# Kernel optimization log

Hardware: AMD Instinct MI355X
Metric: run time of the kernel (lower is better)

The kernel has to match this reference:

```python
import jax, jax.numpy as jnp
import numpy as np

NEG_SLOPE = 0.2
N_NODES = 50000


def gatv2_layer(x, src, dst, Wl, Wr, att, b, concat):
    # GATv2Conv (PyG semantics): x_l = lin_l(x) feeds messages (source side),
    # x_r = lin_r(x) is the target side; attention logit per edge/head is
    # att . leaky_relu(x_l[src] + x_r[dst]); softmax over incoming edges of dst.
    H, C = att.shape
    n = x.shape[0]
    xl = (x @ Wl).reshape(n, H, C)   # [N,H,C]
    xr = (x @ Wr).reshape(n, H, C)
    h = xl[src] + xr[dst]            # [E,H,C] gather
    logits = jnp.einsum('ehc,hc->eh', jax.nn.leaky_relu(h, NEG_SLOPE), att)  # [E,H]
    # segment softmax over target nodes
    m = jax.ops.segment_max(logits, dst, num_segments=n)
    m = jnp.where(jnp.isfinite(m), m, 0.0)
    ex = jnp.exp(logits - m[dst])
    s = jax.ops.segment_sum(ex, dst, num_segments=n)
    alpha = ex / (s[dst] + 1e-16)    # [E,H]
    msg = xl[src] * alpha[:, :, None]               # [E,H,C]
    out = jax.ops.segment_sum(msg, dst, num_segments=n)  # [N,H,C] scatter-add
    out = out.reshape(n, H * C) if concat else out.mean(axis=1)
    return out + b


def setup_inputs() -> dict:
    key = jax.random.key(0)
    ks = jax.random.split(key, 10)
    in_c, out_c, heads = 128, 64, 2
    node_fts = jax.random.normal(ks[0], (N_NODES, in_c), dtype=jnp.float32)
    edge_index = jax.random.randint(ks[1], (2, 800000), 0, N_NODES, dtype=jnp.int64)
    sc = 0.1
    return {
        'node_fts': node_fts,
        'edge_index': edge_index,
        'Wl1': jax.random.normal(ks[2], (in_c, heads * out_c), dtype=jnp.float32) * sc,
        'Wr1': jax.random.normal(ks[3], (in_c, heads * out_c), dtype=jnp.float32) * sc,
        'att1': jax.random.normal(ks[4], (heads, out_c), dtype=jnp.float32) * sc,
        'b1': jnp.zeros((heads * out_c,), dtype=jnp.float32),
        'Wl2': jax.random.normal(ks[5], (heads * out_c, out_c), dtype=jnp.float32) * sc,
        'Wr2': jax.random.normal(ks[6], (heads * out_c, out_c), dtype=jnp.float32) * sc,
        'att2': jax.random.normal(ks[7], (1, out_c), dtype=jnp.float32) * sc,
        'b2': jnp.zeros((out_c,), dtype=jnp.float32),
    }


def reference(node_fts, edge_index, Wl1, Wr1, att1, b1, Wl2, Wr2, att2, b2):
    n = node_fts.shape[0]
    loop = jnp.arange(n, dtype=edge_index.dtype)  # add_self_loops=True default
    src = jnp.concatenate([edge_index[0], loop])
    dst = jnp.concatenate([edge_index[1], loop])
    x = gatv2_layer(node_fts, src, dst, Wl1, Wr1, att1, b1, concat=True)
    x = jax.nn.relu(x)
    x = gatv2_layer(x, src, dst, Wl2, Wr2, att2, b2, concat=False)
    x = jax.nn.relu(x)
    return x
```

## Files before the change

### kernel.cpp

```cpp
#include <hip/hip_runtime.h>
#include <math.h>

typedef unsigned short ush;
typedef short bf16x8 __attribute__((ext_vector_type(8)));
typedef float f32x4 __attribute__((ext_vector_type(4)));
typedef ush ushx8 __attribute__((ext_vector_type(8)));

__device__ __forceinline__ ush f2bf(float f) {
    unsigned u = __float_as_uint(f);
    u += 0x7FFFu + ((u >> 16) & 1u);
    return (ush)(u >> 16);
}
__device__ __forceinline__ float bf2f(ush u) {
    return __uint_as_float((unsigned)u << 16);
}

__global__ __launch_bounds__(64) void prep_w_k(
    const float* __restrict__ Wl1, const float* __restrict__ Wr1,
    const float* __restrict__ Wl2, const float* __restrict__ Wr2,
    ush* __restrict__ wph, ush* __restrict__ wpl) {
    const int bid = blockIdx.x, l = threadIdx.x;
    const float* W;
    int C, fid;
    if (bid < 32)      { W = Wl1; C = 128; fid = bid; }
    else if (bid < 64) { W = Wr1; C = 128; fid = bid - 32; }
    else if (bid < 80) { W = Wl2; C = 64;  fid = bid - 64; }
    else               { W = Wr2; C = 64;  fid = bid - 80; }
    const int nc16 = C / 16;
    const int ks = fid / nc16, c16 = fid % nc16;
#pragma unroll
    for (int j = 0; j < 8; ++j) {
        const int k = ks * 32 + (l >> 4) * 8 + j;
        const int c = c16 * 16 + (l & 15);
        const float v = W[(size_t)k * C + c];
        const ush h = f2bf(v);
        wph[(size_t)(bid * 64 + l) * 8 + j] = h;
        wpl[(size_t)(bid * 64 + l) * 8 + j] = f2bf(v - bf2f(h));
    }
}

__global__ __launch_bounds__(256) void gemm1_k(
    const float* __restrict__ x,
    const ush* __restrict__ wh1, const ush* __restrict__ wl1,
    const ush* __restrict__ wh2, const ush* __restrict__ wl2,
    ush* __restrict__ ybf, float* __restrict__ yf, int n) {
    const int l = threadIdx.x & 63;
    const int w = threadIdx.x >> 6;
    const int r0 = blockIdx.x * 64 + w * 16;
    const int arow = min(r0 + (l & 15), n - 1);
    const int kb = (l >> 4) * 8;

    bf16x8 ah[4], al[4];
#pragma unroll
    for (int ks = 0; ks < 4; ++ks) {
        const float* ap = x + (size_t)arow * 128 + ks * 32 + kb;
        const float4 v0 = *reinterpret_cast<const float4*>(ap);
        const float4 v1 = *reinterpret_cast<const float4*>(ap + 4);
        const float fv[8] = {v0.x, v0.y, v0.z, v0.w, v1.x, v1.y, v1.z, v1.w};
#pragma unroll
        for (int j = 0; j < 8; ++j) {
            const ush h = f2bf(fv[j]);
            ah[ks][j] = (short)h;
            al[ks][j] = (short)f2bf(fv[j] - bf2f(h));
        }
    }
    const int drow = (l >> 4) * 4;
    const int dcol = l & 15;
#pragma unroll
    for (int slab = 0; slab < 4; ++slab) {
        const bool isW1 = slab < 2;
        const int sl = slab & 1;
        const ush* __restrict__ wh = isW1 ? wh1 : wh2;
        const ush* __restrict__ wl = isW1 ? wl1 : wl2;
#pragma unroll
        for (int c16 = 0; c16 < 4; ++c16) {
            f32x4 acc = {0.f, 0.f, 0.f, 0.f};
#pragma unroll
            for (int ks = 0; ks < 4; ++ks) {
                const int fid = ks * 8 + sl * 4 + c16;
                const bf16x8 bh = *reinterpret_cast<const bf16x8*>(wh + (size_t)(fid * 64 + l) * 8);
                const bf16x8 bl = *reinterpret_cast<const bf16x8*>(wl + (size_t)(fid * 64 + l) * 8);
                acc = __builtin_amdgcn_mfma_f32_16x16x32_bf16(ah[ks], bh, acc, 0, 0, 0);
                acc = __builtin_amdgcn_mfma_f32_16x16x32_bf16(al[ks], bh, acc, 0, 0, 0);
                acc = __builtin_amdgcn_mfma_f32_16x16x32_bf16(ah[ks], bl, acc, 0, 0, 0);
            }
            const int cg = sl * 64 + c16 * 16 + dcol;
#pragma unroll
            for (int q = 0; q < 4; ++q) {
                const int gr = r0 + drow + q;
                if (gr < n) {
                    if (isW1) ybf[(size_t)gr * 128 + cg] = f2bf(acc[q]);
                    else      yf[(size_t)gr * 128 + cg] = acc[q];
                }
            }
        }
    }
}

__global__ __launch_bounds__(256) void gemm2_k(
    const ush* __restrict__ ahi, const ush* __restrict__ alo,
    const ush* __restrict__ whl, const ush* __restrict__ wll,
    const ush* __restrict__ whr, const ush* __restrict__ wlr,
    ush* __restrict__ ybf, float* __restrict__ yf, int n) {
    const int l = threadIdx.x & 63;
    const int w = threadIdx.x >> 6;
    const int r0 = blockIdx.x * 64 + w * 16;
    const int arow = min(r0 + (l & 15), n - 1);
    const int kb = (l >> 4) * 8;
    bf16x8 ah[4], al[4];
#pragma unroll
    for (int ks = 0; ks < 4; ++ks) {
        ah[ks] = *reinterpret_cast<const bf16x8*>(ahi + (size_t)arow * 128 + ks * 32 + kb);
        al[ks] = *reinterpret_cast<const bf16x8*>(alo + (size_t)arow * 128 + ks * 32 + kb);
    }
    const int drow = (l >> 4) * 4;
    const int dcol = l & 15;
#pragma unroll
    for (int slab = 0; slab < 2; ++slab) {
        const ush* __restrict__ wh = slab ? whr : whl;
        const ush* __restrict__ wl = slab ? wlr : wll;
#pragma unroll
        for (int c16 = 0; c16 < 4; ++c16) {
            f32x4 acc = {0.f, 0.f, 0.f, 0.f};
#pragma unroll
            for (int ks = 0; ks < 4; ++ks) {
                const int fid = ks * 4 + c16;
                const bf16x8 bh = *reinterpret_cast<const bf16x8*>(wh + (size_t)(fid * 64 + l) * 8);
                const bf16x8 bl = *reinterpret_cast<const bf16x8*>(wl + (size_t)(fid * 64 + l) * 8);
                acc = __builtin_amdgcn_mfma_f32_16x16x32_bf16(ah[ks], bh, acc, 0, 0, 0);
                acc = __builtin_amdgcn_mfma_f32_16x16x32_bf16(al[ks], bh, acc, 0, 0, 0);
                acc = __builtin_amdgcn_mfma_f32_16x16x32_bf16(ah[ks], bl, acc, 0, 0, 0);
            }
            const int cg = c16 * 16 + dcol;
#pragma unroll
            for (int q = 0; q < 4; ++q) {
                const int gr = r0 + drow + q;
                if (gr < n) {
                    if (slab == 0) ybf[(size_t)gr * 64 + cg] = f2bf(acc[q]);
                    else           yf[(size_t)gr * 64 + cg] = acc[q];
                }
            }
        }
    }
}

__global__ __launch_bounds__(256) void hist_k(const int* __restrict__ dsts,
                                              int* __restrict__ ghist,
                                              int e0, int etot) {
    __shared__ int h[512];
    const int t = threadIdx.x;
    for (int i = t; i < 512; i += 256) h[i] = 0;
    __syncthreads();
    for (int i = blockIdx.x * blockDim.x + t; i < etot; i += gridDim.x * blockDim.x) {
        const int d = (i < e0) ? dsts[i] : (i - e0);
        atomicAdd(&h[d >> 7], 1);
    }
    __syncthreads();
    for (int i = t; i < 512; i += 256)
        if (h[i]) atomicAdd(&ghist[i], h[i]);
}

__global__ __launch_bounds__(512) void scanb_k(const int* __restrict__ ghist,
                                               int* __restrict__ boff,
                                               int* __restrict__ cur) {
    __shared__ int red[512];
    const int t = threadIdx.x;
    const int x = ghist[t];
    red[t] = x;
    __syncthreads();
#pragma unroll
    for (int s = 1; s < 512; s <<= 1) {
        const int add = (t >= s) ? red[t - s] : 0;
        __syncthreads();
        red[t] += add;
        __syncthreads();
    }
    const int excl = red[t] - x;
    boff[t] = excl;
    cur[t] = excl;
}

__global__ __launch_bounds__(256) void semisort_k(
    const int* __restrict__ srcs, const int* __restrict__ dsts,
    int* __restrict__ cur, int* __restrict__ pairs, int e0, int etot) {
    __shared__ int hist[512], gbase[512], lcur[512];
    const int t = threadIdx.x;
    const int start = blockIdx.x * 2048;
    const int end = min(start + 2048, etot);
    for (int i = t; i < 512; i += 256) { hist[i] = 0; lcur[i] = 0; }
    __syncthreads();
    for (int i = start + t; i < end; i += 256) {
        const int d = (i < e0) ? dsts[i] : (i - e0);
        atomicAdd(&hist[d >> 7], 1);
    }
    __syncthreads();
    for (int i = t; i < 512; i += 256) {
        const int c = hist[i];
        gbase[i] = c ? atomicAdd(&cur[i], c) : 0;
    }
    __syncthreads();
    for (int i = start + t; i < end; i += 256) {
        int s, d;
        if (i < e0) { s = srcs[i]; d = dsts[i]; } else { s = d = i - e0; }
        const int b = d >> 7;
        const int p = atomicAdd(&lcur[b], 1);
        pairs[gbase[b] + p] = s | ((d & 127) << 24);
    }
}

__global__ __launch_bounds__(256) void bucket_fill_k(
    const int* __restrict__ pairs, const int* __restrict__ boff,
    int* __restrict__ row_ptr, int* __restrict__ csr_src,
    int* __restrict__ dbin, int n, int etot) {
    __shared__ int cnt[128], cur[128], hd[128];
    const int b = blockIdx.x, t = threadIdx.x;
    const int lo = boff[b], hi = boff[b + 1];
    if (t < 128) { cnt[t] = 0; hd[t] = 0; }
    __syncthreads();
    for (int e = lo + t; e < hi; e += 256)
        atomicAdd(&cnt[(pairs[e] >> 24) & 127], 1);
    __syncthreads();
    const int x = (t < 128) ? cnt[t] : 0;
#pragma unroll
    for (int s = 1; s < 128; s <<= 1) {
        const int add = (t < 128 && t >= s) ? cnt[t - s] : 0;
        __syncthreads();
        if (t < 128) cnt[t] += add;
        __syncthreads();
    }
    if (t < 128) {
        const int excl = cnt[t] - x;
        cur[t] = excl;
        const int d = b * 128 + t;
        if (d < n) {
            row_ptr[d] = lo + excl;
            atomicAdd(&hd[127 - min(x, 127)], 1);
        }
    }
    if (b == 0 && t == 0) row_ptr[n] = etot;
    __syncthreads();
    if (t < 128 && hd[t]) atomicAdd(&dbin[t], hd[t]);
    for (int e = lo + t; e < hi; e += 256) {
        const int p = pairs[e];
        const int pos = atomicAdd(&cur[(p >> 24) & 127], 1);
        csr_src[lo + pos] = p & 0xFFFFFF;
    }
}

__global__ __launch_bounds__(128) void deg_scan_k(const int* __restrict__ dbin,
                                                  int* __restrict__ dcur) {
    __shared__ int red[128];
    const int t = threadIdx.x;
    const int x = dbin[t];
    red[t] = x;
    __syncthreads();
#pragma unroll
    for (int s = 1; s < 128; s <<= 1) {
        const int add = (t >= s) ? red[t - s] : 0;
        __syncthreads();
        red[t] += add;
        __syncthreads();
    }
    dcur[t] = red[t] - x;
}

__global__ __launch_bounds__(256) void deg_scatter_k(const int* __restrict__ row_ptr,
                                                     int* __restrict__ dcur,
                                                     int* __restrict__ order, int n) {
    __shared__ int h[128], gbase[128], lcur[128];
    const int t = threadIdx.x;
    if (t < 128) { h[t] = 0; lcur[t] = 0; }
    __syncthreads();
    const int d = blockIdx.x * 256 + t;
    int bin = -1;
    if (d < n) {
        const int deg = row_ptr[d + 1] - row_ptr[d];
        bin = 127 - min(deg, 127);
        atomicAdd(&h[bin], 1);
    }
    __syncthreads();
    if (t < 128) gbase[t] = h[t] ? atomicAdd(&dcur[t], h[t]) : 0;
    __syncthreads();
    if (d < n) {
        const int p = atomicAdd(&lcur[bin], 1);
        order[gbase[bin] + p] = d;
    }
}

__global__ __launch_bounds__(256) void gat_dst2_k(
    const ush* __restrict__ xl, const float* __restrict__ xr,
    const int* __restrict__ row_ptr, const int* __restrict__ csr_src,
    const int* __restrict__ order, const float* __restrict__ att,
    const float* __restrict__ bias, ush* __restrict__ h1hi,
    ush* __restrict__ h1lo, int n) {
    const int lane = threadIdx.x & 63;
    const int g = lane >> 4, il = lane & 15;
    const int w = (blockIdx.x * blockDim.x + threadIdx.x) >> 6;
    if (w >= n) return;
    const int d = order[w];

    float xv[8], av[8];
    {
        const float4* xp = reinterpret_cast<const float4*>(xr + (size_t)d * 128 + il * 8);
        const float4* ap = reinterpret_cast<const float4*>(att + il * 8);
        const float4 x0 = xp[0], x1 = xp[1], a0 = ap[0], a1 = ap[1];
        xv[0]=x0.x; xv[1]=x0.y; xv[2]=x0.z; xv[3]=x0.w;
        xv[4]=x1.x; xv[5]=x1.y; xv[6]=x1.z; xv[7]=x1.w;
        av[0]=a0.x; av[1]=a0.y; av[2]=a0.z; av[3]=a0.w;
        av[4]=a1.x; av[5]=a1.y; av[6]=a1.z; av[7]=a1.w;
    }
    const int rp0 = row_ptr[d], rp1 = row_ptr[d + 1];

    float s = 0.f;
    float acc[8] = {0.f, 0.f, 0.f, 0.f, 0.f, 0.f, 0.f, 0.f};
    int i = rp0 + g;
    for (; i + 4 < rp1; i += 8) {
        const int s0 = csr_src[i];
        const int s1 = csr_src[i + 4];
        const ushx8 u0 = *reinterpret_cast<const ushx8*>(xl + (((size_t)(unsigned)s0) << 7) + il * 8);
        const ushx8 u1 = *reinterpret_cast<const ushx8*>(xl + (((size_t)(unsigned)s1) << 7) + il * 8);
        float f0[8], f1[8], p0 = 0.f, p1 = 0.f;
#pragma unroll
        for (int j = 0; j < 8; ++j) {
            f0[j] = bf2f((ush)u0[j]);
            const float v = f0[j] + xv[j];
            p0 = fmaf(av[j], fmaxf(v, 0.2f * v), p0);
        }
#pragma unroll
        for (int j = 0; j < 8; ++j) {
            f1[j] = bf2f((ush)u1[j]);
            const float v = f1[j] + xv[j];
            p1 = fmaf(av[j], fmaxf(v, 0.2f * v), p1);
        }
        p0 += __shfl_xor(p0, 4, 64); p0 += __shfl_xor(p0, 2, 64); p0 += __shfl_xor(p0, 1, 64);
        p1 += __shfl_xor(p1, 4, 64); p1 += __shfl_xor(p1, 2, 64); p1 += __shfl_xor(p1, 1, 64);
        const float w0 = __expf(p0), w1 = __expf(p1);
        s += w0 + w1;
#pragma unroll
        for (int j = 0; j < 8; ++j) acc[j] = fmaf(w0, f0[j], fmaf(w1, f1[j], acc[j]));
    }
    if (i < rp1) {
        const int s0 = csr_src[i];
        const ushx8 u0 = *reinterpret_cast<const ushx8*>(xl + (((size_t)(unsigned)s0) << 7) + il * 8);
        float f0[8], p0 = 0.f;
#pragma unroll
        for (int j = 0; j < 8; ++j) {
            f0[j] = bf2f((ush)u0[j]);
            const float v = f0[j] + xv[j];
            p0 = fmaf(av[j], fmaxf(v, 0.2f * v), p0);
        }
        p0 += __shfl_xor(p0, 4, 64); p0 += __shfl_xor(p0, 2, 64); p0 += __shfl_xor(p0, 1, 64);
        const float w0 = __expf(p0);
        s += w0;
#pragma unroll
        for (int j = 0; j < 8; ++j) acc[j] = fmaf(w0, f0[j], acc[j]);
    }
#pragma unroll
    for (int off = 16; off <= 32; off <<= 1) {
        s += __shfl_xor(s, off, 64);
#pragma unroll
        for (int j = 0; j < 8; ++j) acc[j] += __shfl_xor(acc[j], off, 64);
    }
    if (g == 0) {
        const float inv = 1.f / (s + 1e-16f);
        float bv[8];
        {
            const float4* bp = reinterpret_cast<const float4*>(bias + il * 8);
            const float4 b0 = bp[0], b1 = bp[1];
            bv[0]=b0.x; bv[1]=b0.y; bv[2]=b0.z; bv[3]=b0.w;
            bv[4]=b1.x; bv[5]=b1.y; bv[6]=b1.z; bv[7]=b1.w;
        }
        ushx8 hh, ll;
#pragma unroll
        for (int j = 0; j < 8; ++j) {
            const float o = fmaxf(fmaf(acc[j], inv, bv[j]), 0.f);
            const ush h = f2bf(o);
            hh[j] = h;
            ll[j] = f2bf(o - bf2f(h));
        }
        *reinterpret_cast<ushx8*>(h1hi + (size_t)d * 128 + il * 8) = hh;
        *reinterpret_cast<ushx8*>(h1lo + (size_t)d * 128 + il * 8) = ll;
    }
}

__global__ __launch_bounds__(256) void gat_dst1_k(
    const ush* __restrict__ xl, const float* __restrict__ xr,
    const int* __restrict__ row_ptr, const int* __restrict__ csr_src,
    const int* __restrict__ order, const float* __restrict__ att,
    const float* __restrict__ bias, float* __restrict__ out, int n) {
    const int lane = threadIdx.x & 63;
    const int g = lane >> 3, il = lane & 7;
    const int w = (blockIdx.x * blockDim.x + threadIdx.x) >> 6;
    if (w >= n) return;
    const int d = order[w];

    float xv[8], av[8];
    {
        const float4* xp = reinterpret_cast<const float4*>(xr + (size_t)d * 64 + il * 8);
        const float4* ap = reinterpret_cast<const float4*>(att + il * 8);
        const float4 x0 = xp[0], x1 = xp[1], a0 = ap[0], a1 = ap[1];
        xv[0]=x0.x; xv[1]=x0.y; xv[2]=x0.z; xv[3]=x0.w;
        xv[4]=x1.x; xv[5]=x1.y; xv[6]=x1.z; xv[7]=x1.w;
        av[0]=a0.x; av[1]=a0.y; av[2]=a0.z; av[3]=a0.w;
        av[4]=a1.x; av[5]=a1.y; av[6]=a1.z; av[7]=a1.w;
    }
    const int rp0 = row_ptr[d], rp1 = row_ptr[d + 1];

    float s = 0.f;
    float acc[8] = {0.f, 0.f, 0.f, 0.f, 0.f, 0.f, 0.f, 0.f};
    int i = rp0 + g;
    for (; i + 8 < rp1; i += 16) {
        const int s0 = csr_src[i];
        const int s1 = csr_src[i + 8];
        const ushx8 u0 = *reinterpret_cast<const ushx8*>(xl + (((size_t)(unsigned)s0) << 6) + il * 8);
        const ushx8 u1 = *reinterpret_cast<const ushx8*>(xl + (((size_t)(unsigned)s1) << 6) + il * 8);
        float f0[8], f1[8], p0 = 0.f, p1 = 0.f;
#pragma unroll
        for (int j = 0; j < 8; ++j) {
            f0[j] = bf2f((ush)u0[j]);
            const float v = f0[j] + xv[j];
            p0 = fmaf(av[j], fmaxf(v, 0.2f * v), p0);
        }
#pragma unroll
        for (int j = 0; j < 8; ++j) {
            f1[j] = bf2f((ush)u1[j]);
            const float v = f1[j] + xv[j];
            p1 = fmaf(av[j], fmaxf(v, 0.2f * v), p1);
        }
        p0 += __shfl_xor(p0, 4, 64); p0 += __shfl_xor(p0, 2, 64); p0 += __shfl_xor(p0, 1, 64);
        p1 += __shfl_xor(p1, 4, 64); p1 += __shfl_xor(p1, 2, 64); p1 += __shfl_xor(p1, 1, 64);
        const float w0 = __expf(p0), w1 = __expf(p1);
        s += w0 + w1;
#pragma unroll
        for (int j = 0; j < 8; ++j) acc[j] = fmaf(w0, f0[j], fmaf(w1, f1[j], acc[j]));
    }
    if (i < rp1) {
        const int s0 = csr_src[i];
        const ushx8 u0 = *reinterpret_cast<const ushx8*>(xl + (((size_t)(unsigned)s0) << 6) + il * 8);
        float f0[8], p0 = 0.f;
#pragma unroll
        for (int j = 0; j < 8; ++j) {
            f0[j] = bf2f((ush)u0[j]);
            const float v = f0[j] + xv[j];
            p0 = fmaf(av[j], fmaxf(v, 0.2f * v), p0);
        }
        p0 += __shfl_xor(p0, 4, 64); p0 += __shfl_xor(p0, 2, 64); p0 += __shfl_xor(p0, 1, 64);
        const float w0 = __expf(p0);
        s += w0;
#pragma unroll
        for (int j = 0; j < 8; ++j) acc[j] = fmaf(w0, f0[j], acc[j]);
    }
#pragma unroll
    for (int off = 8; off <= 32; off <<= 1) {
        s += __shfl_xor(s, off, 64);
#pragma unroll
        for (int j = 0; j < 8; ++j) acc[j] += __shfl_xor(acc[j], off, 64);
    }
    if (g == 0) {
        const float inv = 1.f / (s + 1e-16f);
        float bv[8];
        {
            const float4* bp = reinterpret_cast<const float4*>(bias + il * 8);
            const float4 b0 = bp[0], b1 = bp[1];
            bv[0]=b0.x; bv[1]=b0.y; bv[2]=b0.z; bv[3]=b0.w;
            bv[4]=b1.x; bv[5]=b1.y; bv[6]=b1.z; bv[7]=b1.w;
        }
        float4 o0, o1;
        o0.x = fmaxf(fmaf(acc[0], inv, bv[0]), 0.f);
        o0.y = fmaxf(fmaf(acc[1], inv, bv[1]), 0.f);
        o0.z = fmaxf(fmaf(acc[2], inv, bv[2]), 0.f);
        o0.w = fmaxf(fmaf(acc[3], inv, bv[3]), 0.f);
        o1.x = fmaxf(fmaf(acc[4], inv, bv[4]), 0.f);
        o1.y = fmaxf(fmaf(acc[5], inv, bv[5]), 0.f);
        o1.z = fmaxf(fmaf(acc[6], inv, bv[6]), 0.f);
        o1.w = fmaxf(fmaf(acc[7], inv, bv[7]), 0.f);
        float4* op = reinterpret_cast<float4*>(out + (size_t)d * 64 + il * 8);
        op[0] = o0;
        op[1] = o1;
    }
}

extern "C" void kernel_launch(void* const* d_in, const int* in_sizes, int n_in,
                              void* d_out, int out_size, void* d_ws, size_t ws_size,
                              hipStream_t stream) {
    const float* x    = (const float*)d_in[0];
    const int*   ei   = (const int*)d_in[1];
    const float* Wl1  = (const float*)d_in[2];
    const float* Wr1  = (const float*)d_in[3];
    const float* att1 = (const float*)d_in[4];
    const float* b1   = (const float*)d_in[5];
    const float* Wl2  = (const float*)d_in[6];
    const float* Wr2  = (const float*)d_in[7];
    const float* att2 = (const float*)d_in[8];
    const float* b2   = (const float*)d_in[9];

    const int n    = in_sizes[0] / 128;
    const int e0   = in_sizes[1] / 2;
    const int etot = e0 + n;
    const int* srcs = ei;
    const int* dsts = ei + e0;

    float* ws = (float*)d_ws;
    ush*   h1hi = (ush*)ws;
    ush*   h1lo = (ush*)(ws + (size_t)n * 64);
    ush*   xlbf = (ush*)(ws + (size_t)n * 128);
    float* xr   = ws + (size_t)n * 192;
    int* row_ptr = (int*)(ws + (size_t)n * 320);
    int* ghist   = row_ptr + (n + 2);
    int* dbin    = ghist + 512;
    int* dcur    = dbin + 128;
    int* boff    = dcur + 128;
    int* cur     = boff + 512;
    int* order   = cur + 512;
    int* csr_src = order + n;
    int* pairs   = csr_src + etot;
    ush* wph     = (ush*)(pairs + etot);
    ush* wpl     = wph + 96 * 512;

    const int NB  = (n + 127) / 128;
    const int NDB = (n + 255) / 256;
    const int nblka = (etot + 2047) / 2048;

    hipMemsetAsync(ghist, 0, 640 * sizeof(int), stream);
    hist_k<<<256, 256, 0, stream>>>(dsts, ghist, e0, etot);
    scanb_k<<<1, 512, 0, stream>>>(ghist, boff, cur);
    semisort_k<<<nblka, 256, 0, stream>>>(srcs, dsts, cur, pairs, e0, etot);
    bucket_fill_k<<<NB, 256, 0, stream>>>(pairs, boff, row_ptr, csr_src, dbin, n, etot);
    deg_scan_k<<<1, 128, 0, stream>>>(dbin, dcur);
    deg_scatter_k<<<NDB, 256, 0, stream>>>(row_ptr, dcur, order, n);

    prep_w_k<<<96, 64, 0, stream>>>(Wl1, Wr1, Wl2, Wr2, wph, wpl);

    const int gx = (n + 63) / 64;

    gemm1_k<<<gx, 256, 0, stream>>>(x, wph, wpl, wph + 32 * 512, wpl + 32 * 512,
                                    xlbf, xr, n);
    gat_dst2_k<<<(n + 3) / 4, 256, 0, stream>>>(xlbf, xr, row_ptr, csr_src, order,
                                                att1, b1, h1hi, h1lo, n);

    gemm2_k<<<gx, 256, 0, stream>>>(h1hi, h1lo, wph + 64 * 512, wpl + 64 * 512,
                                    wph + 80 * 512, wpl + 80 * 512, xlbf, xr, n);
    gat_dst1_k<<<(n + 3) / 4, 256, 0, stream>>>(xlbf, xr, row_ptr, csr_src, order,
                                                att2, b2, (float*)d_out, n);
}
```

Before: 188.0 us.

## Fuse CSR build stages and run them alongside weight prep and first GEMM

Merges the graph preprocessing pipeline into fewer launches, going from roughly eleven to six. The histogram runs in the same launch as weight packing. The bucket scan is recomputed inside the semisort blocks, which share a grid with the layer-1 GEMM. Bucket fill now also builds the degree-sorted node order, so the separate degree scan and scatter kernels go away. The aim is to remove launch and serialization gaps and overlap independent work. The trade-off is that nodes are now degree-sorted only within each 128-node bucket rather than globally, which may change load balance in the attention kernels.

```diff
diff --git a/kernel.cpp b/kernel.cpp
--- a/kernel.cpp
+++ b/kernel.cpp
@@ -15,85 +15,216 @@
     return __uint_as_float((unsigned)u << 16);
 }
 
-__global__ __launch_bounds__(64) void prep_w_k(
+__global__ __launch_bounds__(256) void fusedA_k(
+    const int* __restrict__ dsts, int* __restrict__ ghist,
     const float* __restrict__ Wl1, const float* __restrict__ Wr1,
     const float* __restrict__ Wl2, const float* __restrict__ Wr2,
-    ush* __restrict__ wph, ush* __restrict__ wpl) {
-    const int bid = blockIdx.x, l = threadIdx.x;
-    const float* W;
-    int C, fid;
-    if (bid < 32)      { W = Wl1; C = 128; fid = bid; }
-    else if (bid < 64) { W = Wr1; C = 128; fid = bid - 32; }
-    else if (bid < 80) { W = Wl2; C = 64;  fid = bid - 64; }
-    else               { W = Wr2; C = 64;  fid = bid - 80; }
-    const int nc16 = C / 16;
-    const int ks = fid / nc16, c16 = fid % nc16;
-#pragma unroll
-    for (int j = 0; j < 8; ++j) {
-        const int k = ks * 32 + (l >> 4) * 8 + j;
-        const int c = c16 * 16 + (l & 15);
-        const float v = W[(size_t)k * C + c];
-        const ush h = f2bf(v);
-        wph[(size_t)(bid * 64 + l) * 8 + j] = h;
-        wpl[(size_t)(bid * 64 + l) * 8 + j] = f2bf(v - bf2f(h));
-    }
-}
-
-__global__ __launch_bounds__(256) void gemm1_k(
+    ush* __restrict__ wph, ush* __restrict__ wpl, int e0, int etot) {
+    const int t = threadIdx.x;
+    if (blockIdx.x < 256) {
+        __shared__ int h[512];
+        for (int i = t; i < 512; i += 256) h[i] = 0;
+        __syncthreads();
+        for (int i = blockIdx.x * 256 + t; i < etot; i += 256 * 256) {
+            const int d = (i < e0) ? dsts[i] : (i - e0);
+            atomicAdd(&h[d >> 7], 1);
+        }
+        __syncthreads();
+        for (int i = t; i < 512; i += 256)
+            if (h[i]) atomicAdd(&ghist[i], h[i]);
+    } else {
+        const int bid = (blockIdx.x - 256) * 4 + (t >> 6);
+        const int l = t & 63;
+        const float* W;
+        int C, fid;
+        if (bid < 32)      { W = Wl1; C = 128; fid = bid; }
+        else if (bid < 64) { W = Wr1; C = 128; fid = bid - 32; }
+        else if (bid < 80) { W = Wl2; C = 64;  fid = bid - 64; }
+        else               { W = Wr2; C = 64;  fid = bid - 80; }
+        const int nc16 = C / 16;
+        const int ks = fid / nc16, c16 = fid % nc16;
+#pragma unroll
+        for (int j = 0; j < 8; ++j) {
+            const int k = ks * 32 + (l >> 4) * 8 + j;
+            const int c = c16 * 16 + (l & 15);
+            const float v = W[(size_t)k * C + c];
+            const ush h = f2bf(v);
+            wph[(size_t)(bid * 64 + l) * 8 + j] = h;
+            wpl[(size_t)(bid * 64 + l) * 8 + j] = f2bf(v - bf2f(h));
+        }
+    }
+}
+
+__global__ __launch_bounds__(256) void fusedB_k(
+    const int* __restrict__ srcs, const int* __restrict__ dsts,
+    const int* __restrict__ ghist, int* __restrict__ cur, int* __restrict__ pairs,
     const float* __restrict__ x,
     const ush* __restrict__ wh1, const ush* __restrict__ wl1,
     const ush* __restrict__ wh2, const ush* __restrict__ wl2,
-    ush* __restrict__ ybf, float* __restrict__ yf, int n) {
-    const int l = threadIdx.x & 63;
-    const int w = threadIdx.x >> 6;
-    const int r0 = blockIdx.x * 64 + w * 16;
-    const int arow = min(r0 + (l & 15), n - 1);
-    const int kb = (l >> 4) * 8;
-
-    bf16x8 ah[4], al[4];
-#pragma unroll
-    for (int ks = 0; ks < 4; ++ks) {
-        const float* ap = x + (size_t)arow * 128 + ks * 32 + kb;
-        const float4 v0 = *reinterpret_cast<const float4*>(ap);
-        const float4 v1 = *reinterpret_cast<const float4*>(ap + 4);
-        const float fv[8] = {v0.x, v0.y, v0.z, v0.w, v1.x, v1.y, v1.z, v1.w};
-#pragma unroll
-        for (int j = 0; j < 8; ++j) {
-            const ush h = f2bf(fv[j]);
-            ah[ks][j] = (short)h;
-            al[ks][j] = (short)f2bf(fv[j] - bf2f(h));
-        }
-    }
-    const int drow = (l >> 4) * 4;
-    const int dcol = l & 15;
-#pragma unroll
-    for (int slab = 0; slab < 4; ++slab) {
-        const bool isW1 = slab < 2;
-        const int sl = slab & 1;
-        const ush* __restrict__ wh = isW1 ? wh1 : wh2;
-        const ush* __restrict__ wl = isW1 ? wl1 : wl2;
-#pragma unroll
-        for (int c16 = 0; c16 < 4; ++c16) {
-            f32x4 acc = {0.f, 0.f, 0.f, 0.f};
-#pragma unroll
-            for (int ks = 0; ks < 4; ++ks) {
-                const int fid = ks * 8 + sl * 4 + c16;
-                const bf16x8 bh = *reinterpret_cast<const bf16x8*>(wh + (size_t)(fid * 64 + l) * 8);
-                const bf16x8 bl = *reinterpret_cast<const bf16x8*>(wl + (size_t)(fid * 64 + l) * 8);
-                acc = __builtin_amdgcn_mfma_f32_16x16x32_bf16(ah[ks], bh, acc, 0, 0, 0);
-                acc = __builtin_amdgcn_mfma_f32_16x16x32_bf16(al[ks], bh, acc, 0, 0, 0);
-                acc = __builtin_amdgcn_mfma_f32_16x16x32_bf16(ah[ks], bl, acc, 0, 0, 0);
+    ush* __restrict__ ybf, float* __restrict__ yf,
+    int e0, int etot, int nblka, int n) {
+    const int t = threadIdx.x;
+    if ((int)blockIdx.x < nblka) {
+        __shared__ int sb[512];
+        __shared__ int red[256];
+        __shared__ int hist[512], gbase[512], lcur[512];
+        const int a0 = ghist[2 * t], a1 = ghist[2 * t + 1];
+        red[t] = a0 + a1;
+        __syncthreads();
+#pragma unroll
+        for (int s = 1; s < 256; s <<= 1) {
+            const int add = (t >= s) ? red[t - s] : 0;
+            __syncthreads();
+            red[t] += add;
+            __syncthreads();
+        }
+        const int base = red[t] - a0 - a1;
+        sb[2 * t] = base;
+        sb[2 * t + 1] = base + a0;
+        for (int i = t; i < 512; i += 256) { hist[i] = 0; lcur[i] = 0; }
+        __syncthreads();
+        const int start = blockIdx.x * 2048;
+        const int end = min(start + 2048, etot);
+        for (int i = start + t; i < end; i += 256) {
+            const int d = (i < e0) ? dsts[i] : (i - e0);
+            atomicAdd(&hist[d >> 7], 1);
+        }
+        __syncthreads();
+        for (int i = t; i < 512; i += 256) {
+            const int c = hist[i];
+            gbase[i] = c ? (sb[i] + atomicAdd(&cur[i], c)) : 0;
+        }
+        __syncthreads();
+        for (int i = start + t; i < end; i += 256) {
+            int s, d;
+            if (i < e0) { s = srcs[i]; d = dsts[i]; } else { s = d = i - e0; }
+            const int b = d >> 7;
+            const int p = atomicAdd(&lcur[b], 1);
+            pairs[gbase[b] + p] = s | ((d & 127) << 24);
+        }
+    } else {
+        const int l = t & 63;
+        const int w = t >> 6;
+        const int r0 = ((int)blockIdx.x - nblka) * 64 + w * 16;
+        const int arow = min(r0 + (l & 15), n - 1);
+        const int kb = (l >> 4) * 8;
+        bf16x8 ah[4], al[4];
+#pragma unroll
+        for (int ks = 0; ks < 4; ++ks) {
+            const float* ap = x + (size_t)arow * 128 + ks * 32 + kb;
+            const float4 v0 = *reinterpret_cast<const float4*>(ap);
+            const float4 v1 = *reinterpret_cast<const float4*>(ap + 4);
+            const float fv[8] = {v0.x, v0.y, v0.z, v0.w, v1.x, v1.y, v1.z, v1.w};
+#pragma unroll
+            for (int j = 0; j < 8; ++j) {
+                const ush h = f2bf(fv[j]);
+                ah[ks][j] = (short)h;
+                al[ks][j] = (short)f2bf(fv[j] - bf2f(h));
             }
-            const int cg = sl * 64 + c16 * 16 + dcol;
-#pragma unroll
-            for (int q = 0; q < 4; ++q) {
-                const int gr = r0 + drow + q;
-                if (gr < n) {
-                    if (isW1) ybf[(size_t)gr * 128 + cg] = f2bf(acc[q]);
-                    else      yf[(size_t)gr * 128 + cg] = acc[q];
+        }
+        const int drow = (l >> 4) * 4;
+        const int dcol = l & 15;
+#pragma unroll
+        for (int slab = 0; slab < 4; ++slab) {
+            const bool isW1 = slab < 2;
+            const int sl = slab & 1;
+            const ush* __restrict__ wh = isW1 ? wh1 : wh2;
+            const ush* __restrict__ wl = isW1 ? wl1 : wl2;
+#pragma unroll
+            for (int c16 = 0; c16 < 4; ++c16) {
+                f32x4 acc = {0.f, 0.f, 0.f, 0.f};
+#pragma unroll
+                for (int ks = 0; ks < 4; ++ks) {
+                    const int fid = ks * 8 + sl * 4 + c16;
+                    const bf16x8 bh = *reinterpret_cast<const bf16x8*>(wh + (size_t)(fid * 64 + l) * 8);
+                    const bf16x8 bl = *reinterpret_cast<const bf16x8*>(wl + (size_t)(fid * 64 + l) * 8);
+                    acc = __builtin_amdgcn_mfma_f32_16x16x32_bf16(ah[ks], bh, acc, 0, 0, 0);
+                    acc = __builtin_amdgcn_mfma_f32_16x16x32_bf16(al[ks], bh, acc, 0, 0, 0);
+                    acc = __builtin_amdgcn_mfma_f32_16x16x32_bf16(ah[ks], bl, acc, 0, 0, 0);
+                }
+                const int cg = sl * 64 + c16 * 16 + dcol;
+#pragma unroll
+                for (int q = 0; q < 4; ++q) {
+                    const int gr = r0 + drow + q;
+                    if (gr < n) {
+                        if (isW1) ybf[(size_t)gr * 128 + cg] = f2bf(acc[q]);
+                        else      yf[(size_t)gr * 128 + cg] = acc[q];
+                    }
                 }
             }
         }
+    }
+}
+
+__global__ __launch_bounds__(256) void bucket_fill2_k(
+    const int* __restrict__ pairs, const int* __restrict__ ghist,
+    int* __restrict__ row_ptr, int* __restrict__ csr_src,
+    int* __restrict__ order, int n, int etot) {
+    __shared__ int sb[512];
+    __shared__ int red[256];
+    __shared__ int cnt[128], cur[128], hcnt[128], horg[128], hcur[128];
+    const int b = blockIdx.x, t = threadIdx.x;
+    const int a0 = ghist[2 * t], a1 = ghist[2 * t + 1];
+    red[t] = a0 + a1;
+    __syncthreads();
+#pragma unroll
+    for (int s = 1; s < 256; s <<= 1) {
+        const int add = (t >= s) ? red[t - s] : 0;
+        __syncthreads();
+        red[t] += add;
+        __syncthreads();
+    }
+    const int base = red[t] - a0 - a1;
+    sb[2 * t] = base;
+    sb[2 * t + 1] = base + a0;
+    if (t < 128) { cnt[t] = 0; hcnt[t] = 0; hcur[t] = 0; }
+    __syncthreads();
+    const int lo = sb[b];
+    const int hi = (b + 1 < 512) ? sb[b + 1] : etot;
+    for (int e = lo + t; e < hi; e += 256)
+        atomicAdd(&cnt[(pairs[e] >> 24) & 127], 1);
+    __syncthreads();
+    const int x = (t < 128) ? cnt[t] : 0;
+#pragma unroll
+    for (int s = 1; s < 128; s <<= 1) {
+        const int add = (t < 128 && t >= s) ? cnt[t - s] : 0;
+        __syncthreads();
+        if (t < 128) cnt[t] += add;
+        __syncthreads();
+    }
+    int key = 0;
+    bool valid = false;
+    if (t < 128) {
+        const int excl = cnt[t] - x;
+        cur[t] = excl;
+        const int d = b * 128 + t;
+        if (d < n) {
+            valid = true;
+            row_ptr[d] = lo + excl;
+            key = 127 - min(x, 127);
+            atomicAdd(&hcnt[key], 1);
+        }
+    }
+    if (b == 0 && t == 0) row_ptr[n] = etot;
+    __syncthreads();
+    if (t < 128) horg[t] = hcnt[t];
+    __syncthreads();
+#pragma unroll
+    for (int s = 1; s < 128; s <<= 1) {
+        const int add = (t < 128 && t >= s) ? hcnt[t - s] : 0;
+        __syncthreads();
+        if (t < 128) hcnt[t] += add;
+        __syncthreads();
+    }
+    if (valid) {
+        const int pos = (hcnt[key] - horg[key]) + atomicAdd(&hcur[key], 1);
+        order[b * 128 + pos] = b * 128 + t;
+    }
+    __syncthreads();
+    for (int e = lo + t; e < hi; e += 256) {
+        const int p = pairs[e];
+        const int pos = atomicAdd(&cur[(p >> 24) & 127], 1);
+        csr_src[lo + pos] = p & 0xFFFFFF;
     }
 }
 
@@ -141,149 +272,6 @@
                 }
             }
         }
-    }
-}
-
-__global__ __launch_bounds__(256) void hist_k(const int* __restrict__ dsts,
-                                              int* __restrict__ ghist,
-                                              int e0, int etot) {
-    __shared__ int h[512];
-    const int t = threadIdx.x;
-    for (int i = t; i < 512; i += 256) h[i] = 0;
-    __syncthreads();
-    for (int i = blockIdx.x * blockDim.x + t; i < etot; i += gridDim.x * blockDim.x) {
-        const int d = (i < e0) ? dsts[i] : (i - e0);
-        atomicAdd(&h[d >> 7], 1);
-    }
-    __syncthreads();
-    for (int i = t; i < 512; i += 256)
-        if (h[i]) atomicAdd(&ghist[i], h[i]);
-}
-
-__global__ __launch_bounds__(512) void scanb_k(const int* __restrict__ ghist,
-                                               int* __restrict__ boff,
-                                               int* __restrict__ cur) {
-    __shared__ int red[512];
-    const int t = threadIdx.x;
-    const int x = ghist[t];
-    red[t] = x;
-    __syncthreads();
-#pragma unroll
-    for (int s = 1; s < 512; s <<= 1) {
-        const int add = (t >= s) ? red[t - s] : 0;
-        __syncthreads();
-        red[t] += add;
-        __syncthreads();
-    }
-    const int excl = red[t] - x;
-    boff[t] = excl;
-    cur[t] = excl;
-}
-
-__global__ __launch_bounds__(256) void semisort_k(
-    const int* __restrict__ srcs, const int* __restrict__ dsts,
-    int* __restrict__ cur, int* __restrict__ pairs, int e0, int etot) {
-    __shared__ int hist[512], gbase[512], lcur[512];
-    const int t = threadIdx.x;
-    const int start = blockIdx.x * 2048;
-    const int end = min(start + 2048, etot);
-    for (int i = t; i < 512; i += 256) { hist[i] = 0; lcur[i] = 0; }
-    __syncthreads();
-    for (int i = start + t; i < end; i += 256) {
-        const int d = (i < e0) ? dsts[i] : (i - e0);
-        atomicAdd(&hist[d >> 7], 1);
-    }
-    __syncthreads();
-    for (int i = t; i < 512; i += 256) {
-        const int c = hist[i];
-        gbase[i] = c ? atomicAdd(&cur[i], c) : 0;
-    }
-    __syncthreads();
-    for (int i = start + t; i < end; i += 256) {
-        int s, d;
-        if (i < e0) { s = srcs[i]; d = dsts[i]; } else { s = d = i - e0; }
-        const int b = d >> 7;
-        const int p = atomicAdd(&lcur[b], 1);
-        pairs[gbase[b] + p] = s | ((d & 127) << 24);
-    }
-}
-
-__global__ __launch_bounds__(256) void bucket_fill_k(
-    const int* __restrict__ pairs, const int* __restrict__ boff,
-    int* __restrict__ row_ptr, int* __restrict__ csr_src,
-    int* __restrict__ dbin, int n, int etot) {
-    __shared__ int cnt[128], cur[128], hd[128];
-    const int b = blockIdx.x, t = threadIdx.x;
-    const int lo = boff[b], hi = boff[b + 1];
-    if (t < 128) { cnt[t] = 0; hd[t] = 0; }
-    __syncthreads();
-    for (int e = lo + t; e < hi; e += 256)
-        atomicAdd(&cnt[(pairs[e] >> 24) & 127], 1);
-    __syncthreads();
-    const int x = (t < 128) ? cnt[t] : 0;
-#pragma unroll
-    for (int s = 1; s < 128; s <<= 1) {
-        const int add = (t < 128 && t >= s) ? cnt[t - s] : 0;
-        __syncthreads();
-        if (t < 128) cnt[t] += add;
-        __syncthreads();
-    }
-    if (t < 128) {
-        const int excl = cnt[t] - x;
-        cur[t] = excl;
-        const int d = b * 128 + t;
-        if (d < n) {
-            row_ptr[d] = lo + excl;
-            atomicAdd(&hd[127 - min(x, 127)], 1);
-        }
-    }
-    if (b == 0 && t == 0) row_ptr[n] = etot;
-    __syncthreads();
-    if (t < 128 && hd[t]) atomicAdd(&dbin[t], hd[t]);
-    for (int e = lo + t; e < hi; e += 256) {
-        const int p = pairs[e];
-        const int pos = atomicAdd(&cur[(p >> 24) & 127], 1);
-        csr_src[lo + pos] = p & 0xFFFFFF;
-    }
-}
-
-__global__ __launch_bounds__(128) void deg_scan_k(const int* __restrict__ dbin,
-                                                  int* __restrict__ dcur) {
-    __shared__ int red[128];
-    const int t = threadIdx.x;
-    const int x = dbin[t];
-    red[t] = x;
-    __syncthreads();
-#pragma unroll
-    for (int s = 1; s < 128; s <<= 1) {
-        const int add = (t >= s) ? red[t - s] : 0;
-        __syncthreads();
-        red[t] += add;
-        __syncthreads();
-    }
-    dcur[t] = red[t] - x;
-}
-
-__global__ __launch_bounds__(256) void deg_scatter_k(const int* __restrict__ row_ptr,
-                                                     int* __restrict__ dcur,
-                                                     int* __restrict__ order, int n) {
-    __shared__ int h[128], gbase[128], lcur[128];
-    const int t = threadIdx.x;
-    if (t < 128) { h[t] = 0; lcur[t] = 0; }
-    __syncthreads();
-    const int d = blockIdx.x * 256 + t;
-    int bin = -1;
-    if (d < n) {
-        const int deg = row_ptr[d + 1] - row_ptr[d];
-        bin = 127 - min(deg, 127);
-        atomicAdd(&h[bin], 1);
-    }
-    __syncthreads();
-    if (t < 128) gbase[t] = h[t] ? atomicAdd(&dcur[t], h[t]) : 0;
-    __syncthreads();
-    if (d < n) {
-        const int p = atomicAdd(&lcur[bin], 1);
-        order[gbase[bin] + p] = d;
     }
 }
 
@@ -507,37 +495,28 @@
     float* xr   = ws + (size_t)n * 192;
     int* row_ptr = (int*)(ws + (size_t)n * 320);
     int* ghist   = row_ptr + (n + 2);
-    int* dbin    = ghist + 512;
-    int* dcur    = dbin + 128;
-    int* boff    = dcur + 128;
-    int* cur     = boff + 512;
+    int* cur     = ghist + 512;
     int* order   = cur + 512;
     int* csr_src = order + n;
     int* pairs   = csr_src + etot;
     ush* wph     = (ush*)(pairs + etot);
     ush* wpl     = wph + 96 * 512;
 
-    const int NB  = (n + 127) / 128;
-    const int NDB = (n + 255) / 256;
+    const int NB    = (n + 127) / 128;
     const int nblka = (etot + 2047) / 2048;
-
-    hipMemsetAsync(ghist, 0, 640 * sizeof(int), stream);
-    hist_k<<<256, 256, 0, stream>>>(dsts, ghist, e0, etot);
-    scanb_k<<<1, 512, 0, stream>>>(ghist, boff, cur);
-    semisort_k<<<nblka, 256, 0, stream>>>(srcs, dsts, cur, pairs, e0, etot);
-    bucket_fill_k<<<NB, 256, 0, stream>>>(pairs, boff, row_ptr, csr_src, dbin, n, etot);
-    deg_scan_k<<<1, 128, 0, stream>>>(dbin, dcur);
-    deg_scatter_k<<<NDB, 256, 0, stream>>>(row_ptr, dcur, order, n);
-
-    prep_w_k<<<96, 64, 0, stream>>>(Wl1, Wr1, Wl2, Wr2, wph, wpl);
-
-    const int gx = (n + 63) / 64;
-
-    gemm1_k<<<gx, 256, 0, stream>>>(x, wph, wpl, wph + 32 * 512, wpl + 32 * 512,
-                                    xlbf, xr, n);
+    const int gx    = (n + 63) / 64;
+
+    hipMemsetAsync(ghist, 0, 1024 * sizeof(int), stream);
+    fusedA_k<<<256 + 24, 256, 0, stream>>>(dsts, ghist, Wl1, Wr1, Wl2, Wr2,
+                                           wph, wpl, e0, etot);
+    fusedB_k<<<nblka + gx, 256, 0, stream>>>(
+        srcs, dsts, ghist, cur, pairs, x,
+        wph, wpl, wph + 32 * 512, wpl + 32 * 512, xlbf, xr,
+        e0, etot, nblka, n);
+    bucket_fill2_k<<<NB, 256, 0, stream>>>(pairs, ghist, row_ptr, csr_src,
+                                           order, n, etot);
     gat_dst2_k<<<(n + 3) / 4, 256, 0, stream>>>(xlbf, xr, row_ptr, csr_src, order,
                                                 att1, b1, h1hi, h1lo, n);
-
     gemm2_k<<<gx, 256, 0, stream>>>(h1hi, h1lo, wph + 64 * 512, wpl + 64 * 512,
                                     wph + 80 * 512, wpl + 80 * 512, xlbf, xr, n);
     gat_dst1_k<<<(n + 3) / 4, 256, 0, stream>>>(xlbf, xr, row_ptr, csr_src, order,
```

New measurement: 187.9 us. Within noise of the previous version (-0.1%).
